# Kernel tuning notes

Hardware: AMD Instinct MI355X
Metric: run time of the kernel (lower is better)

## Reference

```python
import jax, jax.numpy as jnp
import numpy as np

N_NODES = 100000
N_EDGES = 1600000
D_FEAT = 128
CONV1_OUT = 64
CONV2_OUT = 32


def setup_inputs() -> dict:
    key = jax.random.key(0)
    k1, k2, k3, k4, k5, k6 = jax.random.split(key, 6)
    x = jax.random.normal(k1, (N_NODES, D_FEAT), dtype=jnp.float32)
    edge_row = jax.random.randint(k2, (N_EDGES,), 0, N_NODES, dtype=jnp.int32)
    edge_col = jax.random.randint(k3, (N_EDGES,), 0, N_NODES, dtype=jnp.int32)
    # normalized adjacency values (D^-1/2 A D^-1/2 entries are small positives)
    edge_val = jax.random.uniform(k4, (N_EDGES,), dtype=jnp.float32) / 16.0
    w1 = jax.random.normal(k5, (D_FEAT, CONV1_OUT), dtype=jnp.float32) / np.sqrt(D_FEAT)
    w2 = jax.random.normal(k6, (CONV1_OUT, CONV2_OUT), dtype=jnp.float32) / np.sqrt(CONV1_OUT)
    return {"x": x, "edge_row": edge_row, "edge_col": edge_col,
            "edge_val": edge_val, "w1": w1, "w2": w2}


def _spmm(edge_row, edge_col, edge_val, h):
    # out[i] = sum_{e: row[e]==i} val[e] * h[col[e]]  (sparse A @ h)
    gathered = edge_val[:, None] * h[edge_col]          # [E, F]
    return jax.ops.segment_sum(gathered, edge_row, num_segments=N_NODES)


def reference(x, edge_row, edge_col, edge_val, w1, w2):
    # Layer 1 (shared weights, relu); dropout inactive at inference.
    h = jnp.relu if False else None  # placeholder to keep linter quiet
    h1 = jax.nn.relu(_spmm(edge_row, edge_col, edge_val, x @ w1))   # [N, 64]
    # Layer 2 (per-cluster, identity activation)
    out = _spmm(edge_row, edge_col, edge_val, h1 @ w2)              # [N, 32]
    return out
```

## Files before the change

### kernel.cpp

```cpp
#include <hip/hip_runtime.h>

#define D_FEAT 128
#define C1 64
#define C2 32
#define BROWS 256
#define LOG_BROWS 8
#define BCAP  4608
#define NBMAX 512
#define GSTRIDE 16
#define CHUNK 8192
#define PTHREADS 512
#define EPT (CHUNK / PTHREADS)
#define WPAD 136
#define HPAD 72
#define VSCALE (32767.0f * 16.0f)
#define VDEQ (1.0f / VSCALE)

using bf16x8 = __attribute__((ext_vector_type(8))) __bf16;
using f32x4  = __attribute__((ext_vector_type(4))) float;

__device__ __forceinline__ unsigned short f2bf(float f) {
    unsigned u = __float_as_uint(f);
    u += 0x7fff + ((u >> 16) & 1);
    return (unsigned short)(u >> 16);
}
__device__ __forceinline__ float bflo(unsigned u) {
    return __uint_as_float(u << 16);
}
__device__ __forceinline__ float bfhi(unsigned u) {
    return __uint_as_float(u & 0xffff0000u);
}

__global__ __launch_bounds__(256) void zero_gcur(int* __restrict__ g, int count) {
    int i = blockIdx.x * 256 + threadIdx.x;
    if (i < count) g[i] = 0;
}

__global__ __launch_bounds__(256) void gemm1_mfma(const float* __restrict__ A,
                                                  const float* __restrict__ W,
                                                  unsigned short* __restrict__ C, int n) {
    __shared__ unsigned short wsb[C1][WPAD];
    __shared__ unsigned short xs[64][WPAD];

    const int t    = threadIdx.x;
    const int lane = t & 63;
    const int w    = t >> 6;
    const int row0 = blockIdx.x * 64;

    #pragma unroll
    for (int it = 0; it < 8; ++it) {
        const int nc = t & 63;
        const int k0 = ((t >> 6) + 4 * it) * 4;
        ushort4 o;
        o.x = f2bf(W[(k0 + 0) * C1 + nc]);
        o.y = f2bf(W[(k0 + 1) * C1 + nc]);
        o.z = f2bf(W[(k0 + 2) * C1 + nc]);
        o.w = f2bf(W[(k0 + 3) * C1 + nc]);
        *(ushort4*)&wsb[nc][k0] = o;
    }

    #pragma unroll
    for (int it = 0; it < 8; ++it) {
        const int qi = it * 256 + t;
        const int r  = qi >> 5;
        const int kq = (qi & 31) * 4;
        const int gr = row0 + r;
        float4 v = make_float4(0.f, 0.f, 0.f, 0.f);
        if (gr < n)
            v = *(const float4*)(A + (size_t)gr * D_FEAT + kq);
        ushort4 o;
        o.x = f2bf(v.x); o.y = f2bf(v.y); o.z = f2bf(v.z); o.w = f2bf(v.w);
        *(ushort4*)&xs[r][kq] = o;
    }
    __syncthreads();

    f32x4 acc[4];
    #pragma unroll
    for (int ct = 0; ct < 4; ++ct)
        acc[ct] = (f32x4){0.f, 0.f, 0.f, 0.f};

    const int mr = w * 16 + (lane & 15);
    const int kq = (lane >> 4) * 8;
    #pragma unroll
    for (int ks = 0; ks < 4; ++ks) {
        bf16x8 av = *(const bf16x8*)&xs[mr][ks * 32 + kq];
        #pragma unroll
        for (int ct = 0; ct < 4; ++ct) {
            bf16x8 bv = *(const bf16x8*)&wsb[ct * 16 + (lane & 15)][ks * 32 + kq];
            acc[ct] = __builtin_amdgcn_mfma_f32_16x16x32_bf16(av, bv, acc[ct], 0, 0, 0);
        }
    }

    const int rowbase = row0 + w * 16 + (lane >> 4) * 4;
    #pragma unroll
    for (int j = 0; j < 4; ++j) {
        const int gr = rowbase + j;
        if (gr < n) {
            #pragma unroll
            for (int ct = 0; ct < 4; ++ct)
                C[(size_t)gr * C1 + ct * 16 + (lane & 15)] = f2bf(acc[ct][j]);
        }
    }
}

__global__ __launch_bounds__(PTHREADS) void partition_kernel(const int* __restrict__ row,
                                                             const int* __restrict__ col,
                                                             const float* __restrict__ val,
                                                             int* __restrict__ gcur,
                                                             int2* __restrict__ bucket,
                                                             int E, int nb) {
    __shared__ int hist[NBMAX];
    __shared__ int base[NBMAX];
    __shared__ int cnt[NBMAX];
    const int t = threadIdx.x;
    const long long e0 = (long long)blockIdx.x * CHUNK;

    for (int i = t; i < nb; i += PTHREADS) {
        hist[i] = 0;
        cnt[i] = 0;
    }
    __syncthreads();

    int r[EPT];
    #pragma unroll
    for (int k = 0; k < EPT; k++) {
        long long i = e0 + k * PTHREADS + t;
        r[k] = (i < E) ? row[i] : -1;
        if (r[k] >= 0) atomicAdd(&hist[r[k] >> LOG_BROWS], 1);
    }
    __syncthreads();

    for (int i = t; i < nb; i += PTHREADS)
        if (hist[i] > 0)
            base[i] = atomicAdd(&gcur[i * GSTRIDE], hist[i]);
    __syncthreads();

    #pragma unroll
    for (int k = 0; k < EPT; k++) {
        long long i = e0 + k * PTHREADS + t;
        if (r[k] >= 0) {
            int b = r[k] >> LOG_BROWS;
            int off = base[b] + atomicAdd(&cnt[b], 1);
            if (off < BCAP)
                bucket[(size_t)b * BCAP + off] =
                    make_int2(((r[k] & (BROWS - 1)) << 17) | col[i], __float_as_int(val[i]));
        }
    }
}

__global__ __launch_bounds__(512) void bucket_scan(const int* __restrict__ gcur,
                                                   int* __restrict__ bstart, int nb) {
    __shared__ int s[512];
    const int t = threadIdx.x;
    int v = (t < nb) ? gcur[t * GSTRIDE] : 0;
    s[t] = v;
    __syncthreads();
    for (int off = 1; off < 512; off <<= 1) {
        int x = (t >= off) ? s[t - off] : 0;
        __syncthreads();
        s[t] += x;
        __syncthreads();
    }
    if (t < nb) bstart[t] = s[t] - v;
}

__global__ __launch_bounds__(256) void bucket_place(const int* __restrict__ gcur,
                                                    const int* __restrict__ bstart,
                                                    const int2* __restrict__ bucket,
                                                    int* __restrict__ ptr,
                                                    unsigned* __restrict__ csr, int n) {
    __shared__ int rhist[BROWS];
    __shared__ int rcur[BROWS];
    __shared__ int sscan[BROWS];
    __shared__ unsigned lbuf[BCAP];
    const int b = blockIdx.x;
    const int t = threadIdx.x;
    const int cnt = min(gcur[b * GSTRIDE], BCAP);
    const int gbase = bstart[b];
    const int2* bb = bucket + (size_t)b * BCAP;

    rhist[t] = 0;
    __syncthreads();

    for (int j = t; j < cnt; j += 256)
        atomicAdd(&rhist[bb[j].x >> 17], 1);
    __syncthreads();

    const int v = rhist[t];
    sscan[t] = v;
    __syncthreads();
    for (int off = 1; off < 256; off <<= 1) {
        int x = (t >= off) ? sscan[t - off] : 0;
        __syncthreads();
        sscan[t] += x;
        __syncthreads();
    }
    const int excl = sscan[t] - v;
    rcur[t] = excl;
    const int r0 = b * BROWS + t;
    if (r0 < n) ptr[r0] = gbase + excl;
    __syncthreads();

    for (int j = t; j < cnt; j += 256) {
        int2 w = bb[j];
        int lr = w.x >> 17;
        int pos = atomicAdd(&rcur[lr], 1);
        float fv = __int_as_float(w.y);
        unsigned vq = (unsigned)__float2int_rn(fv * VSCALE);
        vq = min(vq, 32767u);
        lbuf[pos] = ((unsigned)(w.x & 0x1FFFF) << 15) | vq;
    }
    __syncthreads();

    for (int j = t; j < cnt; j += 256)
        csr[(size_t)gbase + j] = lbuf[j];
}

__global__ __launch_bounds__(256) void spmm64_fused(const int* __restrict__ ptr,
                                                    const unsigned* __restrict__ csr,
                                                    const uint4* __restrict__ Hb,
                                                    const float* __restrict__ W2,
                                                    unsigned short* __restrict__ Zb,
                                                    int n, int E) {
    __shared__ unsigned short hlds[32][HPAD];
    __shared__ unsigned short w2t[C2][HPAD];

    const int t    = threadIdx.x;
    const int lane = t & 63;
    const int w    = t >> 6;
    const int g    = lane >> 3;
    const int lp   = lane & 7;
    const int rloc = w * 8 + g;
    const int row  = blockIdx.x * 32 + rloc;

    {
        const int nc = t & 31;
        const int k0 = (t >> 5) * 8;
        #pragma unroll
        for (int i = 0; i < 8; ++i)
            w2t[nc][k0 + i] = f2bf(W2[(k0 + i) * C2 + nc]);
    }

    int start = 0, end = 0;
    if (row < n) {
        start = ptr[row];
        end   = (row + 1 < n) ? ptr[row + 1] : E;
    }

    float A0 = 0.f, A1 = 0.f, A2 = 0.f, A3 = 0.f;
    float A4 = 0.f, A5 = 0.f, A6 = 0.f, A7 = 0.f;
    int e = start;
    for (; e + 7 < end; e += 8) {
        unsigned c[8];
        uint4 G[8];
        #pragma unroll
        for (int q = 0; q < 8; q++) c[q] = __builtin_nontemporal_load(&csr[e + q]);
        #pragma unroll
        for (int q = 0; q < 8; q++) G[q] = Hb[(size_t)(c[q] >> 15) * 8 + lp];
        #pragma unroll
        for (int q = 0; q < 8; q++) {
            float v = (float)(c[q] & 0x7FFF) * VDEQ;
            A0 += v * bflo(G[q].x); A1 += v * bfhi(G[q].x);
            A2 += v * bflo(G[q].y); A3 += v * bfhi(G[q].y);
            A4 += v * bflo(G[q].z); A5 += v * bfhi(G[q].z);
            A6 += v * bflo(G[q].w); A7 += v * bfhi(G[q].w);
        }
    }
    if (e + 3 < end) {
        unsigned c[4];
        uint4 G[4];
        #pragma unroll
        for (int q = 0; q < 4; q++) c[q] = __builtin_nontemporal_load(&csr[e + q]);
        #pragma unroll
        for (int q = 0; q < 4; q++) G[q] = Hb[(size_t)(c[q] >> 15) * 8 + lp];
        #pragma unroll
        for (int q = 0; q < 4; q++) {
            float v = (float)(c[q] & 0x7FFF) * VDEQ;
            A0 += v * bflo(G[q].x); A1 += v * bfhi(G[q].x);
            A2 += v * bflo(G[q].y); A3 += v * bfhi(G[q].y);
            A4 += v * bflo(G[q].z); A5 += v * bfhi(G[q].z);
            A6 += v * bflo(G[q].w); A7 += v * bfhi(G[q].w);
        }
        e += 4;
    }
    for (; e < end; e++) {
        unsigned c = __builtin_nontemporal_load(&csr[e]);
        uint4 gg = Hb[(size_t)(c >> 15) * 8 + lp];
        float v = (float)(c & 0x7FFF) * VDEQ;
        A0 += v * bflo(gg.x); A1 += v * bfhi(gg.x);
        A2 += v * bflo(gg.y); A3 += v * bfhi(gg.y);
        A4 += v * bflo(gg.z); A5 += v * bfhi(gg.z);
        A6 += v * bflo(gg.w); A7 += v * bfhi(gg.w);
    }

    {
        ushort4 o0, o1;
        o0.x = f2bf(fmaxf(A0, 0.f)); o0.y = f2bf(fmaxf(A1, 0.f));
        o0.z = f2bf(fmaxf(A2, 0.f)); o0.w = f2bf(fmaxf(A3, 0.f));
        o1.x = f2bf(fmaxf(A4, 0.f)); o1.y = f2bf(fmaxf(A5, 0.f));
        o1.z = f2bf(fmaxf(A6, 0.f)); o1.w = f2bf(fmaxf(A7, 0.f));
        *(ushort4*)&hlds[rloc][lp * 8]     = o0;
        *(ushort4*)&hlds[rloc][lp * 8 + 4] = o1;
    }
    __syncthreads();

    if (w < 2) {
        f32x4 acc[2];
        acc[0] = (f32x4){0.f, 0.f, 0.f, 0.f};
        acc[1] = (f32x4){0.f, 0.f, 0.f, 0.f};
        const int kq = (lane >> 4) * 8;
        #pragma unroll
        for (int ks = 0; ks < 2; ++ks) {
            bf16x8 av = *(const bf16x8*)&hlds[w * 16 + (lane & 15)][ks * 32 + kq];
            #pragma unroll
            for (int ct = 0; ct < 2; ++ct) {
                bf16x8 bv = *(const bf16x8*)&w2t[ct * 16 + (lane & 15)][ks * 32 + kq];
                acc[ct] = __builtin_amdgcn_mfma_f32_16x16x32_bf16(av, bv, acc[ct], 0, 0, 0);
            }
        }
        #pragma unroll
        for (int j = 0; j < 4; ++j) {
            const int grow = blockIdx.x * 32 + w * 16 + (lane >> 4) * 4 + j;
            if (grow < n) {
                #pragma unroll
                for (int ct = 0; ct < 2; ++ct)
                    Zb[(size_t)grow * C2 + ct * 16 + (lane & 15)] = f2bf(acc[ct][j]);
            }
        }
    }
}

__global__ __launch_bounds__(256) void spmm_csr32(const int* __restrict__ ptr,
                                                  const unsigned* __restrict__ csr,
                                                  const uint2* __restrict__ Zb,
                                                  float* __restrict__ OUT, int n, int E) {
    const int tid  = blockIdx.x * 256 + threadIdx.x;
    const int gwid = tid >> 6;
    const int lane = threadIdx.x & 63;
    const int g    = lane >> 3;
    const int lp   = lane & 7;
    const int row  = gwid * 8 + g;

    int start = 0, end = 0;
    if (row < n) {
        start = ptr[row];
        end   = (row + 1 < n) ? ptr[row + 1] : E;
    }

    float a0 = 0.f, a1 = 0.f, a2 = 0.f, a3 = 0.f;
    int e = start;
    for (; e + 7 < end; e += 8) {
        unsigned c[8];
        uint2 G[8];
        #pragma unroll
        for (int q = 0; q < 8; q++) c[q] = __builtin_nontemporal_load(&csr[e + q]);
        #pragma unroll
        for (int q = 0; q < 8; q++) G[q] = Zb[(size_t)(c[q] >> 15) * 8 + lp];
        #pragma unroll
        for (int q = 0; q < 8; q++) {
            float v = (float)(c[q] & 0x7FFF) * VDEQ;
            a0 += v * bflo(G[q].x); a1 += v * bfhi(G[q].x);
            a2 += v * bflo(G[q].y); a3 += v * bfhi(G[q].y);
        }
    }
    if (e + 3 < end) {
        unsigned c[4];
        uint2 G[4];
        #pragma unroll
        for (int q = 0; q < 4; q++) c[q] = __builtin_nontemporal_load(&csr[e + q]);
        #pragma unroll
        for (int q = 0; q < 4; q++) G[q] = Zb[(size_t)(c[q] >> 15) * 8 + lp];
        #pragma unroll
        for (int q = 0; q < 4; q++) {
            float v = (float)(c[q] & 0x7FFF) * VDEQ;
            a0 += v * bflo(G[q].x); a1 += v * bfhi(G[q].x);
            a2 += v * bflo(G[q].y); a3 += v * bfhi(G[q].y);
        }
        e += 4;
    }
    for (; e < end; e++) {
        unsigned c = __builtin_nontemporal_load(&csr[e]);
        uint2 gg = Zb[(size_t)(c >> 15) * 8 + lp];
        float v = (float)(c & 0x7FFF) * VDEQ;
        a0 += v * bflo(gg.x); a1 += v * bfhi(gg.x);
        a2 += v * bflo(gg.y); a3 += v * bfhi(gg.y);
    }
    if (row < n)
        *(float4*)(OUT + (size_t)row * C2 + 4 * lp) = make_float4(a0, a1, a2, a3);
}

extern "C" void kernel_launch(void* const* d_in, const int* in_sizes, int n_in,
                              void* d_out, int out_size, void* d_ws, size_t ws_size,
                              hipStream_t stream) {
    const float* x    = (const float*)d_in[0];
    const int*   erow = (const int*)d_in[1];
    const int*   ecol = (const int*)d_in[2];
    const float* eval = (const float*)d_in[3];
    const float* w1   = (const float*)d_in[4];
    const float* w2   = (const float*)d_in[5];
    float* out = (float*)d_out;

    const int n = in_sizes[0] / D_FEAT;
    const int E = in_sizes[1];

    const int nb = (n + BROWS - 1) / BROWS;
    const int pblocks = (E + CHUNK - 1) / CHUNK;

    unsigned short* y1b = (unsigned short*)d_ws;
    int2*  bucket = (int2*)(y1b + (size_t)n * C1);
    unsigned* csr = (unsigned*)(bucket + (size_t)nb * BCAP);
    int*   ptr    = (int*)(csr + E);
    int*   gcur   = ptr + n + 64;
    int*   bstart = gcur + NBMAX * GSTRIDE;
    unsigned short* zb = (unsigned short*)(bstart + NBMAX);

    {
        int count = nb * GSTRIDE;
        zero_gcur<<<(count + 255) / 256, 256, 0, stream>>>(gcur, count);
    }
    partition_kernel<<<pblocks, PTHREADS, 0, stream>>>(erow, ecol, eval, gcur, bucket, E, nb);
    bucket_scan<<<1, 512, 0, stream>>>(gcur, bstart, nb);
    bucket_place<<<nb, 256, 0, stream>>>(gcur, bstart, bucket, ptr, csr, n);

    gemm1_mfma<<<(n + 63) / 64, 256, 0, stream>>>(x, w1, y1b, n);

    spmm64_fused<<<(n + 31) / 32, 256, 0, stream>>>(ptr, csr, (const uint4*)y1b,
                                                    w2, zb, n, E);

    {
        int rows_per_block = 32;
        int blocks = (n + rows_per_block - 1) / rows_per_block;
        spmm_csr32<<<blocks, 256, 0, stream>>>(ptr, csr, (const uint2*)zb,
                                               out, n, E);
    }
}
```

Before: 120.6 us.

## Merge edge partitioning and GEMM1 into one heterogeneous kernel launch

Combines the partition kernel and the first dense GEMM into a single launch whose blocks branch on block index, sharing LDS through a union. GEMM blocks now cover 128 rows with 512 threads. The aim is to overlap the two independent stages and save one launch. The partition phase now rereads row indices from global memory instead of keeping them in registers, and the CSR loads in both SpMM kernels switch from nontemporal to regular loads, which may change cache behaviour.

```diff
diff --git a/kernel.cpp b/kernel.cpp
--- a/kernel.cpp
+++ b/kernel.cpp
@@ -9,8 +9,8 @@
 #define NBMAX 512
 #define GSTRIDE 16
 #define CHUNK 8192
-#define PTHREADS 512
-#define EPT (CHUNK / PTHREADS)
+#define PT 512
+#define EPT (CHUNK / PT)
 #define WPAD 136
 #define HPAD 72
 #define VSCALE (32767.0f * 16.0f)
@@ -36,114 +36,114 @@
     if (i < count) g[i] = 0;
 }
 
-__global__ __launch_bounds__(256) void gemm1_mfma(const float* __restrict__ A,
-                                                  const float* __restrict__ W,
-                                                  unsigned short* __restrict__ C, int n) {
-    __shared__ unsigned short wsb[C1][WPAD];
-    __shared__ unsigned short xs[64][WPAD];
-
-    const int t    = threadIdx.x;
-    const int lane = t & 63;
-    const int w    = t >> 6;
-    const int row0 = blockIdx.x * 64;
-
-    #pragma unroll
-    for (int it = 0; it < 8; ++it) {
-        const int nc = t & 63;
-        const int k0 = ((t >> 6) + 4 * it) * 4;
-        ushort4 o;
-        o.x = f2bf(W[(k0 + 0) * C1 + nc]);
-        o.y = f2bf(W[(k0 + 1) * C1 + nc]);
-        o.z = f2bf(W[(k0 + 2) * C1 + nc]);
-        o.w = f2bf(W[(k0 + 3) * C1 + nc]);
-        *(ushort4*)&wsb[nc][k0] = o;
-    }
-
-    #pragma unroll
-    for (int it = 0; it < 8; ++it) {
-        const int qi = it * 256 + t;
-        const int r  = qi >> 5;
-        const int kq = (qi & 31) * 4;
-        const int gr = row0 + r;
-        float4 v = make_float4(0.f, 0.f, 0.f, 0.f);
-        if (gr < n)
-            v = *(const float4*)(A + (size_t)gr * D_FEAT + kq);
-        ushort4 o;
-        o.x = f2bf(v.x); o.y = f2bf(v.y); o.z = f2bf(v.z); o.w = f2bf(v.w);
-        *(ushort4*)&xs[r][kq] = o;
-    }
-    __syncthreads();
-
-    f32x4 acc[4];
-    #pragma unroll
-    for (int ct = 0; ct < 4; ++ct)
-        acc[ct] = (f32x4){0.f, 0.f, 0.f, 0.f};
-
-    const int mr = w * 16 + (lane & 15);
-    const int kq = (lane >> 4) * 8;
-    #pragma unroll
-    for (int ks = 0; ks < 4; ++ks) {
-        bf16x8 av = *(const bf16x8*)&xs[mr][ks * 32 + kq];
-        #pragma unroll
-        for (int ct = 0; ct < 4; ++ct) {
-            bf16x8 bv = *(const bf16x8*)&wsb[ct * 16 + (lane & 15)][ks * 32 + kq];
-            acc[ct] = __builtin_amdgcn_mfma_f32_16x16x32_bf16(av, bv, acc[ct], 0, 0, 0);
-        }
-    }
-
-    const int rowbase = row0 + w * 16 + (lane >> 4) * 4;
-    #pragma unroll
-    for (int j = 0; j < 4; ++j) {
-        const int gr = rowbase + j;
-        if (gr < n) {
+union PartGemmSM {
+    struct { int hist[NBMAX]; int base[NBMAX]; int cnt[NBMAX]; } p;
+    struct { unsigned short wsb[C1][WPAD]; unsigned short xs[128][WPAD]; } g;
+};
+
+__global__ __launch_bounds__(PT) void part_gemm1(const int* __restrict__ row,
+                                                 const int* __restrict__ col,
+                                                 const float* __restrict__ val,
+                                                 int* __restrict__ gcur,
+                                                 int2* __restrict__ bucket,
+                                                 const float* __restrict__ A,
+                                                 const float* __restrict__ W,
+                                                 unsigned short* __restrict__ C,
+                                                 int E, int nb, int n, int pblocks) {
+    __shared__ PartGemmSM sm;
+    const int t = threadIdx.x;
+
+    if ((int)blockIdx.x < pblocks) {
+        const long long e0 = (long long)blockIdx.x * CHUNK;
+        for (int i = t; i < nb; i += PT) {
+            sm.p.hist[i] = 0;
+            sm.p.cnt[i] = 0;
+        }
+        __syncthreads();
+
+        #pragma unroll
+        for (int k = 0; k < EPT; k++) {
+            long long i = e0 + (long long)k * PT + t;
+            if (i < E) atomicAdd(&sm.p.hist[row[i] >> LOG_BROWS], 1);
+        }
+        __syncthreads();
+
+        for (int i = t; i < nb; i += PT)
+            if (sm.p.hist[i] > 0)
+                sm.p.base[i] = atomicAdd(&gcur[i * GSTRIDE], sm.p.hist[i]);
+        __syncthreads();
+
+        #pragma unroll
+        for (int k = 0; k < EPT; k++) {
+            long long i = e0 + (long long)k * PT + t;
+            if (i < E) {
+                int rr = row[i];
+                int b = rr >> LOG_BROWS;
+                int off = sm.p.base[b] + atomicAdd(&sm.p.cnt[b], 1);
+                if (off < BCAP)
+                    bucket[(size_t)b * BCAP + off] =
+                        make_int2(((rr & (BROWS - 1)) << 17) | col[i],
+                                  __float_as_int(val[i]));
+            }
+        }
+    } else {
+        const int lane = t & 63;
+        const int w    = t >> 6;
+        const int row0 = ((int)blockIdx.x - pblocks) * 128;
+
+        #pragma unroll
+        for (int it = 0; it < 4; ++it) {
+            const int nc = t & 63;
+            const int k0 = ((t >> 6) + 8 * it) * 4;
+            ushort4 o;
+            o.x = f2bf(W[(k0 + 0) * C1 + nc]);
+            o.y = f2bf(W[(k0 + 1) * C1 + nc]);
+            o.z = f2bf(W[(k0 + 2) * C1 + nc]);
+            o.w = f2bf(W[(k0 + 3) * C1 + nc]);
+            *(ushort4*)&sm.g.wsb[nc][k0] = o;
+        }
+
+        #pragma unroll
+        for (int it = 0; it < 8; ++it) {
+            const int qi = it * PT + t;
+            const int r  = qi >> 5;
+            const int kq = (qi & 31) * 4;
+            const int gr = row0 + r;
+            float4 v = make_float4(0.f, 0.f, 0.f, 0.f);
+            if (gr < n)
+                v = *(const float4*)(A + (size_t)gr * D_FEAT + kq);
+            ushort4 o;
+            o.x = f2bf(v.x); o.y = f2bf(v.y); o.z = f2bf(v.z); o.w = f2bf(v.w);
+            *(ushort4*)&sm.g.xs[r][kq] = o;
+        }
+        __syncthreads();
+
+        f32x4 acc[4];
+        #pragma unroll
+        for (int ct = 0; ct < 4; ++ct)
+            acc[ct] = (f32x4){0.f, 0.f, 0.f, 0.f};
+
+        const int mr = w * 16 + (lane & 15);
+        const int kq = (lane >> 4) * 8;
+        #pragma unroll
+        for (int ks = 0; ks < 4; ++ks) {
+            bf16x8 av = *(const bf16x8*)&sm.g.xs[mr][ks * 32 + kq];
             #pragma unroll
-            for (int ct = 0; ct < 4; ++ct)
-                C[(size_t)gr * C1 + ct * 16 + (lane & 15)] = f2bf(acc[ct][j]);
-        }
-    }
-}
-
-__global__ __launch_bounds__(PTHREADS) void partition_kernel(const int* __restrict__ row,
-                                                             const int* __restrict__ col,
-                                                             const float* __restrict__ val,
-                                                             int* __restrict__ gcur,
-                                                             int2* __restrict__ bucket,
-                                                             int E, int nb) {
-    __shared__ int hist[NBMAX];
-    __shared__ int base[NBMAX];
-    __shared__ int cnt[NBMAX];
-    const int t = threadIdx.x;
-    const long long e0 = (long long)blockIdx.x * CHUNK;
-
-    for (int i = t; i < nb; i += PTHREADS) {
-        hist[i] = 0;
-        cnt[i] = 0;
-    }
-    __syncthreads();
-
-    int r[EPT];
-    #pragma unroll
-    for (int k = 0; k < EPT; k++) {
-        long long i = e0 + k * PTHREADS + t;
-        r[k] = (i < E) ? row[i] : -1;
-        if (r[k] >= 0) atomicAdd(&hist[r[k] >> LOG_BROWS], 1);
-    }
-    __syncthreads();
-
-    for (int i = t; i < nb; i += PTHREADS)
-        if (hist[i] > 0)
-            base[i] = atomicAdd(&gcur[i * GSTRIDE], hist[i]);
-    __syncthreads();
-
-    #pragma unroll
-    for (int k = 0; k < EPT; k++) {
-        long long i = e0 + k * PTHREADS + t;
-        if (r[k] >= 0) {
-            int b = r[k] >> LOG_BROWS;
-            int off = base[b] + atomicAdd(&cnt[b], 1);
-            if (off < BCAP)
-                bucket[(size_t)b * BCAP + off] =
-                    make_int2(((r[k] & (BROWS - 1)) << 17) | col[i], __float_as_int(val[i]));
+            for (int ct = 0; ct < 4; ++ct) {
+                bf16x8 bv = *(const bf16x8*)&sm.g.wsb[ct * 16 + (lane & 15)][ks * 32 + kq];
+                acc[ct] = __builtin_amdgcn_mfma_f32_16x16x32_bf16(av, bv, acc[ct], 0, 0, 0);
+            }
+        }
+
+        const int rowbase = row0 + w * 16 + (lane >> 4) * 4;
+        #pragma unroll
+        for (int j = 0; j < 4; ++j) {
+            const int gr = rowbase + j;
+            if (gr < n) {
+                #pragma unroll
+                for (int ct = 0; ct < 4; ++ct)
+                    C[(size_t)gr * C1 + ct * 16 + (lane & 15)] = f2bf(acc[ct][j]);
+            }
         }
     }
 }
@@ -254,7 +254,7 @@
         unsigned c[8];
         uint4 G[8];
         #pragma unroll
-        for (int q = 0; q < 8; q++) c[q] = __builtin_nontemporal_load(&csr[e + q]);
+        for (int q = 0; q < 8; q++) c[q] = csr[e + q];
         #pragma unroll
         for (int q = 0; q < 8; q++) G[q] = Hb[(size_t)(c[q] >> 15) * 8 + lp];
         #pragma unroll
@@ -270,7 +270,7 @@
         unsigned c[4];
         uint4 G[4];
         #pragma unroll
-        for (int q = 0; q < 4; q++) c[q] = __builtin_nontemporal_load(&csr[e + q]);
+        for (int q = 0; q < 4; q++) c[q] = csr[e + q];
         #pragma unroll
         for (int q = 0; q < 4; q++) G[q] = Hb[(size_t)(c[q] >> 15) * 8 + lp];
         #pragma unroll
@@ -284,7 +284,7 @@
         e += 4;
     }
     for (; e < end; e++) {
-        unsigned c = __builtin_nontemporal_load(&csr[e]);
+        unsigned c = csr[e];
         uint4 gg = Hb[(size_t)(c >> 15) * 8 + lp];
         float v = (float)(c & 0x7FFF) * VDEQ;
         A0 += v * bflo(gg.x); A1 += v * bfhi(gg.x);
@@ -353,7 +353,7 @@
         unsigned c[8];
         uint2 G[8];
         #pragma unroll
-        for (int q = 0; q < 8; q++) c[q] = __builtin_nontemporal_load(&csr[e + q]);
+        for (int q = 0; q < 8; q++) c[q] = csr[e + q];
         #pragma unroll
         for (int q = 0; q < 8; q++) G[q] = Zb[(size_t)(c[q] >> 15) * 8 + lp];
         #pragma unroll
@@ -367,7 +367,7 @@
         unsigned c[4];
         uint2 G[4];
         #pragma unroll
-        for (int q = 0; q < 4; q++) c[q] = __builtin_nontemporal_load(&csr[e + q]);
+        for (int q = 0; q < 4; q++) c[q] = csr[e + q];
         #pragma unroll
         for (int q = 0; q < 4; q++) G[q] = Zb[(size_t)(c[q] >> 15) * 8 + lp];
         #pragma unroll
@@ -379,7 +379,7 @@
         e += 4;
     }
     for (; e < end; e++) {
-        unsigned c = __builtin_nontemporal_load(&csr[e]);
+        unsigned c = csr[e];
         uint2 gg = Zb[(size_t)(c >> 15) * 8 + lp];
         float v = (float)(c & 0x7FFF) * VDEQ;
         a0 += v * bflo(gg.x); a1 += v * bfhi(gg.x);
@@ -405,6 +405,7 @@
 
     const int nb = (n + BROWS - 1) / BROWS;
     const int pblocks = (E + CHUNK - 1) / CHUNK;
+    const int gblocks = (n + 127) / 128;
 
     unsigned short* y1b = (unsigned short*)d_ws;
     int2*  bucket = (int2*)(y1b + (size_t)n * C1);
@@ -418,11 +419,10 @@
         int count = nb * GSTRIDE;
         zero_gcur<<<(count + 255) / 256, 256, 0, stream>>>(gcur, count);
     }
-    partition_kernel<<<pblocks, PTHREADS, 0, stream>>>(erow, ecol, eval, gcur, bucket, E, nb);
+    part_gemm1<<<pblocks + gblocks, PT, 0, stream>>>(erow, ecol, eval, gcur, bucket,
+                                                     x, w1, y1b, E, nb, n, pblocks);
     bucket_scan<<<1, 512, 0, stream>>>(gcur, bstart, nb);
     bucket_place<<<nb, 256, 0, stream>>>(gcur, bstart, bucket, ptr, csr, n);
-
-    gemm1_mfma<<<(n + 63) / 64, 256, 0, stream>>>(x, w1, y1b, n);
 
     spmm64_fused<<<(n + 31) / 32, 256, 0, stream>>>(ptr, csr, (const uint4*)y1b,
                                                     w2, zb, n, E);
```

After: 108.9 us. 9.7% less time.
